# Kernel optimization log

Measured on AMD Instinct MI355X. Metric: run time of the kernel, lower is better.

The kernel has to match this reference:

```python
import jax, jax.numpy as jnp
import numpy as np

N_NODES = 100000
N_EDGES = 1600000
D_IN = 128
HID = 128
E_CH = 16


def setup_inputs() -> dict:
    key = jax.random.key(0)
    ks = jax.random.split(key, 16)

    def glorot(k, shape):
        fan_in, fan_out = shape[0], shape[1]
        lim = jnp.sqrt(6.0 / (fan_in + fan_out))
        return jax.random.uniform(k, shape, jnp.float32, -lim, lim)

    inp = {
        "x": jax.random.normal(ks[0], (N_NODES, D_IN), jnp.float32),
        "edge_index": jax.random.randint(ks[1], (2, N_EDGES), 0, N_NODES, jnp.int32),
        "edge_attr": jax.random.normal(ks[2], (N_EDGES, E_CH), jnp.float32),
        # SAGEConv layer 0: lin_l (neighbor agg, with bias), lin_r (root, no bias)
        "Wl0": glorot(ks[3], (D_IN, HID)),
        "Wr0": glorot(ks[4], (D_IN, HID)),
        "b0": jnp.zeros((HID,), jnp.float32),
        # SAGEConv layer 1
        "Wl1": glorot(ks[5], (HID, HID)),
        "Wr1": glorot(ks[6], (HID, HID)),
        "b1": jnp.zeros((HID,), jnp.float32),
        # classifier MLP: (2*HID + E_CH) -> 128 -> 64 -> 1
        "Wc1": glorot(ks[7], (2 * HID + E_CH, 128)),
        "bc1": jnp.zeros((128,), jnp.float32),
        "Wc2": glorot(ks[8], (128, 64)),
        "bc2": jnp.zeros((64,), jnp.float32),
        "Wc3": glorot(ks[9], (64, 1)),
        "bc3": jnp.zeros((1,), jnp.float32),
    }
    return inp


def _sage_conv(x, src, dst, Wl, Wr, b):
    # PyG SAGEConv (aggr='mean'): out = lin_l(mean_j x_j) + lin_r(x_i)
    # messages flow src -> dst
    msg_sum = jax.ops.segment_sum(x[src], dst, num_segments=N_NODES)  # [N, D]
    deg = jax.ops.segment_sum(jnp.ones((src.shape[0],), x.dtype), dst,
                              num_segments=N_NODES)                   # [N]
    agg = msg_sum / jnp.maximum(deg, 1.0)[:, None]  # mean; isolated nodes -> 0
    return agg @ Wl + b + x @ Wr


def reference(x, edge_index, edge_attr,
              Wl0, Wr0, b0, Wl1, Wr1, b1,
              Wc1, bc1, Wc2, bc2, Wc3, bc3):
    src, dst = edge_index[0], edge_index[1]
    # encode: two SAGEConv layers, each followed by ReLU (dropout is identity at eval)
    h = jax.nn.relu(_sage_conv(x, src, dst, Wl0, Wr0, b0))
    h = jax.nn.relu(_sage_conv(h, src, dst, Wl1, Wr1, b1))
    # edge classifier: gather endpoint embeddings, concat edge features
    feat = jnp.concatenate([h[src], h[dst], edge_attr], axis=-1)  # [E, 2H+EC]
    z = jax.nn.relu(feat @ Wc1 + bc1)
    z = jax.nn.relu(z @ Wc2 + bc2)
    logits = (z @ Wc3 + bc3).reshape(-1)  # [E]
    return jax.nn.sigmoid(logits)
```

## Files before the change

kernel.cpp:

```cpp
#include <hip/hip_runtime.h>
#include <hip/hip_bf16.h>
#include <math.h>

#define NN 100000
#define NE 1600000
#define NBLK 391

typedef __bf16 bf16x8 __attribute__((ext_vector_type(8)));
typedef float f32x4 __attribute__((ext_vector_type(4)));

union BF8 { bf16x8 v; unsigned short u[8]; };

static __device__ __forceinline__ unsigned short f2bf(float f) {
  unsigned int u = __float_as_uint(f);
  unsigned int r = u + 0x7fffu + ((u >> 16) & 1u);
  return (unsigned short)(r >> 16);
}
static __device__ __forceinline__ f32x4 zero4() {
  f32x4 z = {0.f, 0.f, 0.f, 0.f}; return z;
}
static __device__ __forceinline__ bf16x8 zerobf8() {
  BF8 t;
  #pragma unroll
  for (int j = 0; j < 8; ++j) t.u[j] = 0;
  return t.v;
}
static __device__ __forceinline__ bf16x8 cvt8(float4 v0, float4 v1, float s) {
  BF8 t;
  t.u[0]=f2bf(v0.x*s); t.u[1]=f2bf(v0.y*s); t.u[2]=f2bf(v0.z*s); t.u[3]=f2bf(v0.w*s);
  t.u[4]=f2bf(v1.x*s); t.u[5]=f2bf(v1.y*s); t.u[6]=f2bf(v1.z*s); t.u[7]=f2bf(v1.w*s);
  return t.v;
}

__global__ void prep_swizzle(const float* __restrict__ Wl0, const float* __restrict__ Wr0,
                             const float* __restrict__ Wl1, const float* __restrict__ Wr1,
                             const float* __restrict__ Wc1, const float* __restrict__ Wc2,
                             __hip_bfloat16* __restrict__ swz) {
  int gid = blockIdx.x * 256 + threadIdx.x;
  if (gid >= 110592) return;
  int id = gid;
  const float* A; const float* B = nullptr; int KC, Nc, Ksrc;
  if (id < 32768)        { KC = 8; Nc = 128; Ksrc = 256; A = Wl0; B = Wr0; }
  else if (id < 65536)   { id -= 32768; KC = 8; Nc = 128; Ksrc = 256; A = Wl1; B = Wr1; }
  else if (id < 102400)  { id -= 65536; KC = 9; Nc = 128; Ksrc = 272; A = Wc1; }
  else                   { id -= 102400; KC = 4; Nc = 64;  Ksrc = 128; A = Wc2; }
  int j = id & 7, lane = (id >> 3) & 63, rest = id >> 9;
  int c = rest % KC, t = rest / KC;
  int k = c * 32 + (lane >> 4) * 8 + j;
  int n = t * 16 + (lane & 15);
  float v = 0.f;
  if (k < Ksrc) {
    if (B && k >= 128) v = B[(k - 128) * Nc + n];
    else               v = A[k * Nc + n];
  }
  unsigned short* o = (unsigned short*)swz;
  o[gid] = f2bf(v);
}

__global__ void deg_count(const int* __restrict__ ei, int* __restrict__ degCnt) {
  int e = blockIdx.x * 256 + threadIdx.x;
  atomicAdd(&degCnt[ei[NE + e]], 1);
}

__global__ void scan_block_sums(const int* __restrict__ degCnt, int* __restrict__ blockSums) {
  __shared__ int red[4];
  int i = blockIdx.x * 256 + threadIdx.x;
  int v = (i < NN) ? degCnt[i] : 0;
  #pragma unroll
  for (int off = 32; off; off >>= 1) v += __shfl_down(v, off, 64);
  if ((threadIdx.x & 63) == 0) red[threadIdx.x >> 6] = v;
  __syncthreads();
  if (threadIdx.x == 0) blockSums[blockIdx.x] = red[0] + red[1] + red[2] + red[3];
}

__global__ void scan_partials(const int* __restrict__ blockSums, int* __restrict__ blockOff) {
  __shared__ int lds[512];
  int t = threadIdx.x;
  int v = (t < NBLK) ? blockSums[t] : 0;
  lds[t] = v; __syncthreads();
  #pragma unroll
  for (int off = 1; off < 512; off <<= 1) {
    int a = (t >= off) ? lds[t - off] : 0;
    __syncthreads();
    lds[t] += a;
    __syncthreads();
  }
  if (t < NBLK) blockOff[t] = lds[t] - v;
}

__global__ void scan_write(const int* __restrict__ degCnt, const int* __restrict__ blockOff,
                           int* __restrict__ rowPtr, int* __restrict__ cursor) {
  __shared__ int lds[256];
  int t = threadIdx.x;
  int i = blockIdx.x * 256 + t;
  int v = (i < NN) ? degCnt[i] : 0;
  lds[t] = v; __syncthreads();
  #pragma unroll
  for (int off = 1; off < 256; off <<= 1) {
    int a = (t >= off) ? lds[t - off] : 0;
    __syncthreads();
    lds[t] += a;
    __syncthreads();
  }
  if (i < NN) {
    int excl = blockOff[blockIdx.x] + lds[t] - v;
    rowPtr[i] = excl;
    cursor[i] = excl;
  }
}

__global__ void csr_fill(const int* __restrict__ ei, int* __restrict__ cursor,
                         int* __restrict__ csrSrc) {
  int e = blockIdx.x * 256 + threadIdx.x;
  int s = ei[e], d = ei[NE + e];
  int idx = atomicAdd(&cursor[d], 1);
  csrSrc[idx] = s;
}

__global__ __launch_bounds__(256, 8)
void gather_agg(const float* __restrict__ xf, const __hip_bfloat16* __restrict__ xb,
                const int* __restrict__ csrSrc, const int* __restrict__ rowPtr,
                const int* __restrict__ degCnt, __hip_bfloat16* __restrict__ msgOut) {
  int n = blockIdx.x * 4 + (threadIdx.x >> 6);
  int c2 = threadIdx.x & 63;
  if (n >= NN) return;
  int rp = rowPtr[n], dg = degCnt[n];
  float acc0 = 0.f, acc1 = 0.f;
  if (xf) {
    for (int i = 0; i < dg; ++i) {
      int s = csrSrc[rp + i];
      float2 v = *(const float2*)(xf + (size_t)s * 128 + c2 * 2);
      acc0 += v.x; acc1 += v.y;
    }
  } else {
    for (int i = 0; i < dg; ++i) {
      int s = csrSrc[rp + i];
      unsigned int u = *(const unsigned int*)(xb + (size_t)s * 128 + c2 * 2);
      acc0 += __uint_as_float(u << 16);
      acc1 += __uint_as_float(u & 0xffff0000u);
    }
  }
  float r = 1.f / fmaxf((float)dg, 1.f);
  unsigned int p = (unsigned int)f2bf(acc0 * r) | ((unsigned int)f2bf(acc1 * r) << 16);
  *(unsigned int*)((unsigned short*)msgOut + (size_t)n * 128 + c2 * 2) = p;
}

__global__ __launch_bounds__(256, 2)
void node_gemm(const __hip_bfloat16* __restrict__ msgB,
               const float* __restrict__ selfF32, const __hip_bfloat16* __restrict__ selfB16,
               const __hip_bfloat16* __restrict__ swzW, const float* __restrict__ bias,
               __hip_bfloat16* __restrict__ hOut) {
  const int tid = threadIdx.x, w = tid >> 6, lane = tid & 63;
  const int l15 = lane & 15, quad = lane >> 4;
  const int nBase = blockIdx.x * 256 + w * 64;

  int row[4];
  #pragma unroll
  for (int t = 0; t < 4; ++t) {
    int n = nBase + t * 16 + l15;
    if (n > NN - 1) n = NN - 1;
    row[t] = n;
  }

  f32x4 acc[8][4];
  #pragma unroll
  for (int mt = 0; mt < 8; ++mt)
    #pragma unroll
    for (int nt = 0; nt < 4; ++nt) acc[mt][nt] = zero4();

  #pragma unroll
  for (int c = 0; c < 8; ++c) {
    bf16x8 bfr[4];
    if (c < 4) {
      #pragma unroll
      for (int nt = 0; nt < 4; ++nt)
        bfr[nt] = *(const bf16x8*)(msgB + (size_t)row[nt] * 128 + c * 32 + quad * 8);
    } else {
      int cc = (c - 4) * 32 + quad * 8;
      if (selfF32) {
        #pragma unroll
        for (int nt = 0; nt < 4; ++nt) {
          const float4* p = (const float4*)(selfF32 + (size_t)row[nt] * 128 + cc);
          bfr[nt] = cvt8(p[0], p[1], 1.f);
        }
      } else {
        #pragma unroll
        for (int nt = 0; nt < 4; ++nt)
          bfr[nt] = *(const bf16x8*)(selfB16 + (size_t)row[nt] * 128 + cc);
      }
    }
    bf16x8 afr[8];
    #pragma unroll
    for (int mt = 0; mt < 8; ++mt)
      afr[mt] = *(const bf16x8*)(swzW + ((mt * 8 + c) * 64 + lane) * 8);
    #pragma unroll
    for (int mt = 0; mt < 8; ++mt)
      #pragma unroll
      for (int nt = 0; nt < 4; ++nt)
        acc[mt][nt] = __builtin_amdgcn_mfma_f32_16x16x32_bf16(afr[mt], bfr[nt], acc[mt][nt], 0, 0, 0);
  }

  #pragma unroll
  for (int mt = 0; mt < 8; ++mt) {
    const float4 b4 = *(const float4*)(bias + mt * 16 + quad * 4);
    #pragma unroll
    for (int nt = 0; nt < 4; ++nt) {
      int n = nBase + nt * 16 + l15;
      if (n < NN) {
        ushort4 p;
        p.x = f2bf(fmaxf(acc[mt][nt][0] + b4.x, 0.f));
        p.y = f2bf(fmaxf(acc[mt][nt][1] + b4.y, 0.f));
        p.z = f2bf(fmaxf(acc[mt][nt][2] + b4.z, 0.f));
        p.w = f2bf(fmaxf(acc[mt][nt][3] + b4.w, 0.f));
        *(ushort4*)(hOut + (size_t)n * 128 + mt * 16 + quad * 4) = p;
      }
    }
  }
}

__global__ __launch_bounds__(256, 2)
void edge_mlp(const __hip_bfloat16* __restrict__ h1, const int* __restrict__ ei,
              const float* __restrict__ ea,
              const __hip_bfloat16* __restrict__ swzWc1, const __hip_bfloat16* __restrict__ swzWc2,
              const float* __restrict__ Wc3, const float* __restrict__ bc1,
              const float* __restrict__ bc2, const float* __restrict__ bc3,
              float* __restrict__ out) {
  __shared__ char lds[4 * 64 * 288];
  const int tid = threadIdx.x, w = tid >> 6, lane = tid & 63;
  const int l15 = lane & 15, quad = lane >> 4;
  const int eBase = blockIdx.x * 256 + w * 64;
  char* zbuf = lds + w * (64 * 288);

  int eRow[4], srcOff[4], dstOff[4];
  #pragma unroll
  for (int t = 0; t < 4; ++t) {
    int e = eBase + t * 16 + l15;
    eRow[t] = e;
    srcOff[t] = ei[e] * 128;
    dstOff[t] = ei[NE + e] * 128;
  }

  f32x4 acc[8][4];
  #pragma unroll
  for (int mt = 0; mt < 8; ++mt)
    #pragma unroll
    for (int nt = 0; nt < 4; ++nt) acc[mt][nt] = zero4();

  #pragma unroll
  for (int c = 0; c < 9; ++c) {
    bf16x8 bfr[4];
    if (c < 4) {
      #pragma unroll
      for (int nt = 0; nt < 4; ++nt)
        bfr[nt] = *(const bf16x8*)(h1 + srcOff[nt] + c * 32 + quad * 8);
    } else if (c < 8) {
      #pragma unroll
      for (int nt = 0; nt < 4; ++nt)
        bfr[nt] = *(const bf16x8*)(h1 + dstOff[nt] + (c - 4) * 32 + quad * 8);
    } else {
      #pragma unroll
      for (int nt = 0; nt < 4; ++nt) {
        if (quad < 2) {
          const float4* p = (const float4*)(ea + (size_t)eRow[nt] * 16 + quad * 8);
          bfr[nt] = cvt8(p[0], p[1], 1.f);
        } else {
          bfr[nt] = zerobf8();
        }
      }
    }
    bf16x8 afr[8];
    #pragma unroll
    for (int mt = 0; mt < 8; ++mt)
      afr[mt] = *(const bf16x8*)(swzWc1 + ((mt * 9 + c) * 64 + lane) * 8);
    #pragma unroll
    for (int mt = 0; mt < 8; ++mt)
      #pragma unroll
      for (int nt = 0; nt < 4; ++nt)
        acc[mt][nt] = __builtin_amdgcn_mfma_f32_16x16x32_bf16(afr[mt], bfr[nt], acc[mt][nt], 0, 0, 0);
  }

  #pragma unroll
  for (int mt = 0; mt < 8; ++mt) {
    const float4 b4 = *(const float4*)(bc1 + mt * 16 + quad * 4);
    #pragma unroll
    for (int nt = 0; nt < 4; ++nt) {
      int er = nt * 16 + l15;
      ushort4 p;
      p.x = f2bf(fmaxf(acc[mt][nt][0] + b4.x, 0.f));
      p.y = f2bf(fmaxf(acc[mt][nt][1] + b4.y, 0.f));
      p.z = f2bf(fmaxf(acc[mt][nt][2] + b4.z, 0.f));
      p.w = f2bf(fmaxf(acc[mt][nt][3] + b4.w, 0.f));
      *(ushort4*)(zbuf + er * 288 + (mt * 16 + quad * 4) * 2) = p;
    }
  }

  f32x4 acc2[4][4];
  #pragma unroll
  for (int mt = 0; mt < 4; ++mt)
    #pragma unroll
    for (int nt = 0; nt < 4; ++nt) acc2[mt][nt] = zero4();

  #pragma unroll
  for (int c = 0; c < 4; ++c) {
    bf16x8 bfr[4];
    #pragma unroll
    for (int nt = 0; nt < 4; ++nt)
      bfr[nt] = *(const bf16x8*)(zbuf + (nt * 16 + l15) * 288 + (c * 32 + quad * 8) * 2);
    bf16x8 afr[4];
    #pragma unroll
    for (int mt = 0; mt < 4; ++mt)
      afr[mt] = *(const bf16x8*)(swzWc2 + ((mt * 4 + c) * 64 + lane) * 8);
    #pragma unroll
    for (int mt = 0; mt < 4; ++mt)
      #pragma unroll
      for (int nt = 0; nt < 4; ++nt)
        acc2[mt][nt] = __builtin_amdgcn_mfma_f32_16x16x32_bf16(afr[mt], bfr[nt], acc2[mt][nt], 0, 0, 0);
  }

  #pragma unroll
  for (int mt = 0; mt < 4; ++mt) {
    const float4 b4 = *(const float4*)(bc2 + mt * 16 + quad * 4);
    #pragma unroll
    for (int nt = 0; nt < 4; ++nt) {
      int er = nt * 16 + l15;
      ushort4 p;
      p.x = f2bf(fmaxf(acc2[mt][nt][0] + b4.x, 0.f));
      p.y = f2bf(fmaxf(acc2[mt][nt][1] + b4.y, 0.f));
      p.z = f2bf(fmaxf(acc2[mt][nt][2] + b4.z, 0.f));
      p.w = f2bf(fmaxf(acc2[mt][nt][3] + b4.w, 0.f));
      *(ushort4*)(zbuf + er * 272 + (mt * 16 + quad * 4) * 2) = p;
    }
  }

  float a3 = bc3[0];
  #pragma unroll
  for (int k2 = 0; k2 < 32; ++k2) {
    unsigned int u = *(const unsigned int*)(zbuf + lane * 272 + k2 * 4);
    float v0 = __uint_as_float(u << 16);
    float v1 = __uint_as_float(u & 0xffff0000u);
    a3 += v0 * Wc3[2 * k2] + v1 * Wc3[2 * k2 + 1];
  }
  out[eBase + lane] = 1.f / (1.f + __expf(-a3));
}

extern "C" void kernel_launch(void* const* d_in, const int* in_sizes, int n_in,
                              void* d_out, int out_size, void* d_ws, size_t ws_size,
                              hipStream_t stream) {
  const float* x   = (const float*)d_in[0];
  const int*   ei  = (const int*)d_in[1];
  const float* ea  = (const float*)d_in[2];
  const float* Wl0 = (const float*)d_in[3];
  const float* Wr0 = (const float*)d_in[4];
  const float* b0  = (const float*)d_in[5];
  const float* Wl1 = (const float*)d_in[6];
  const float* Wr1 = (const float*)d_in[7];
  const float* b1  = (const float*)d_in[8];
  const float* Wc1 = (const float*)d_in[9];
  const float* bc1 = (const float*)d_in[10];
  const float* Wc2 = (const float*)d_in[11];
  const float* bc2 = (const float*)d_in[12];
  const float* Wc3 = (const float*)d_in[13];
  const float* bc3 = (const float*)d_in[14];
  float* out = (float*)d_out;

  char* ws = (char*)d_ws;
  int* degCnt   = (int*)(ws + 0);
  int* rowPtr   = (int*)(ws + 400000);
  int* cursor   = (int*)(ws + 800000);
  int* blockSums= (int*)(ws + 1200000);
  int* blockOff = (int*)(ws + 1202048);
  int* csrSrc   = (int*)(ws + 1204096);
  __hip_bfloat16* msgB = (__hip_bfloat16*)(ws + 7604096);
  __hip_bfloat16* h0b  = (__hip_bfloat16*)(ws + 33204096);
  __hip_bfloat16* h1b  = (__hip_bfloat16*)(ws + 58804096);
  __hip_bfloat16* swz  = (__hip_bfloat16*)(ws + 84404096);

  hipMemsetAsync(degCnt, 0, 400000, stream);
  prep_swizzle<<<432, 256, 0, stream>>>(Wl0, Wr0, Wl1, Wr1, Wc1, Wc2, swz);

  deg_count<<<NE / 256, 256, 0, stream>>>(ei, degCnt);
  scan_block_sums<<<NBLK, 256, 0, stream>>>(degCnt, blockSums);
  scan_partials<<<1, 512, 0, stream>>>(blockSums, blockOff);
  scan_write<<<NBLK, 256, 0, stream>>>(degCnt, blockOff, rowPtr, cursor);
  csr_fill<<<NE / 256, 256, 0, stream>>>(ei, cursor, csrSrc);

  gather_agg<<<NN / 4, 256, 0, stream>>>(x, nullptr, csrSrc, rowPtr, degCnt, msgB);
  node_gemm<<<(NN + 255) / 256, 256, 0, stream>>>(msgB, x, nullptr, swz, b0, h0b);

  gather_agg<<<NN / 4, 256, 0, stream>>>(nullptr, h0b, csrSrc, rowPtr, degCnt, msgB);
  node_gemm<<<(NN + 255) / 256, 256, 0, stream>>>(msgB, nullptr, h0b, swz + 32768, b1, h1b);

  edge_mlp<<<NE / 256, 256, 0, stream>>>(h1b, ei, ea, swz + 65536, swz + 102400,
                                         Wc3, bc1, bc2, bc3, out);
}
```

Before: 1.010 ms.

## Convert x to bf16 up front, split gather across half-waves, shrink edge MLP tiles

Adds a pre-pass that converts x to bf16 so the first gather and the root GEMM read half the bytes. The gather now has each half-wave walk alternate neighbours with 4-channel loads, then combines the halves with a shuffle, which doubles the loads in flight per node. The edge MLP processes 32 edges per wave instead of 64, which cuts accumulator registers so occupancy can rise from 2 to 4 blocks. It also pads the LDS row stride to reduce bank conflicts and splits the final dot product across half-waves. In exchange it adds an extra kernel pass over x and rounds x to bf16 before the first aggregation, and the h1 buffer is reused for the converted x.

```diff
diff --git a/kernel.cpp b/kernel.cpp
--- a/kernel.cpp
+++ b/kernel.cpp
@@ -5,6 +5,7 @@
 #define NN 100000
 #define NE 1600000
 #define NBLK 391
+#define ZSTRIDE 296
 
 typedef __bf16 bf16x8 __attribute__((ext_vector_type(8)));
 typedef float f32x4 __attribute__((ext_vector_type(4)));
@@ -57,6 +58,14 @@
   o[gid] = f2bf(v);
 }
 
+__global__ void x_to_bf16(const float* __restrict__ x, __hip_bfloat16* __restrict__ xb) {
+  int i = blockIdx.x * 256 + threadIdx.x;
+  float4 v = ((const float4*)x)[i];
+  ushort4 p;
+  p.x = f2bf(v.x); p.y = f2bf(v.y); p.z = f2bf(v.z); p.w = f2bf(v.w);
+  ((ushort4*)xb)[i] = p;
+}
+
 __global__ void deg_count(const int* __restrict__ ei, int* __restrict__ degCnt) {
   int e = blockIdx.x * 256 + threadIdx.x;
   atomicAdd(&degCnt[ei[NE + e]], 1);
@@ -118,36 +127,40 @@
 }
 
 __global__ __launch_bounds__(256, 8)
-void gather_agg(const float* __restrict__ xf, const __hip_bfloat16* __restrict__ xb,
+void gather_agg(const __hip_bfloat16* __restrict__ xb,
                 const int* __restrict__ csrSrc, const int* __restrict__ rowPtr,
                 const int* __restrict__ degCnt, __hip_bfloat16* __restrict__ msgOut) {
   int n = blockIdx.x * 4 + (threadIdx.x >> 6);
-  int c2 = threadIdx.x & 63;
+  int lane = threadIdx.x & 63;
+  int half = lane >> 5;
+  int c4 = lane & 31;
   if (n >= NN) return;
   int rp = rowPtr[n], dg = degCnt[n];
-  float acc0 = 0.f, acc1 = 0.f;
-  if (xf) {
-    for (int i = 0; i < dg; ++i) {
-      int s = csrSrc[rp + i];
-      float2 v = *(const float2*)(xf + (size_t)s * 128 + c2 * 2);
-      acc0 += v.x; acc1 += v.y;
-    }
-  } else {
-    for (int i = 0; i < dg; ++i) {
-      int s = csrSrc[rp + i];
-      unsigned int u = *(const unsigned int*)(xb + (size_t)s * 128 + c2 * 2);
-      acc0 += __uint_as_float(u << 16);
-      acc1 += __uint_as_float(u & 0xffff0000u);
-    }
-  }
-  float r = 1.f / fmaxf((float)dg, 1.f);
-  unsigned int p = (unsigned int)f2bf(acc0 * r) | ((unsigned int)f2bf(acc1 * r) << 16);
-  *(unsigned int*)((unsigned short*)msgOut + (size_t)n * 128 + c2 * 2) = p;
+  float a0 = 0.f, a1 = 0.f, a2 = 0.f, a3 = 0.f;
+  for (int i = half; i < dg; i += 2) {
+    int s = csrSrc[rp + i];
+    uint2 u = *(const uint2*)((const unsigned short*)xb + (size_t)s * 128 + c4 * 4);
+    a0 += __uint_as_float(u.x << 16);
+    a1 += __uint_as_float(u.x & 0xffff0000u);
+    a2 += __uint_as_float(u.y << 16);
+    a3 += __uint_as_float(u.y & 0xffff0000u);
+  }
+  a0 += __shfl_xor(a0, 32);
+  a1 += __shfl_xor(a1, 32);
+  a2 += __shfl_xor(a2, 32);
+  a3 += __shfl_xor(a3, 32);
+  if (half == 0) {
+    float r = 1.f / fmaxf((float)dg, 1.f);
+    ushort4 p;
+    p.x = f2bf(a0 * r); p.y = f2bf(a1 * r);
+    p.z = f2bf(a2 * r); p.w = f2bf(a3 * r);
+    *(ushort4*)((unsigned short*)msgOut + (size_t)n * 128 + c4 * 4) = p;
+  }
 }
 
 __global__ __launch_bounds__(256, 2)
 void node_gemm(const __hip_bfloat16* __restrict__ msgB,
-               const float* __restrict__ selfF32, const __hip_bfloat16* __restrict__ selfB16,
+               const __hip_bfloat16* __restrict__ selfB16,
                const __hip_bfloat16* __restrict__ swzW, const float* __restrict__ bias,
                __hip_bfloat16* __restrict__ hOut) {
   const int tid = threadIdx.x, w = tid >> 6, lane = tid & 63;
@@ -176,18 +189,9 @@
       for (int nt = 0; nt < 4; ++nt)
         bfr[nt] = *(const bf16x8*)(msgB + (size_t)row[nt] * 128 + c * 32 + quad * 8);
     } else {
-      int cc = (c - 4) * 32 + quad * 8;
-      if (selfF32) {
-        #pragma unroll
-        for (int nt = 0; nt < 4; ++nt) {
-          const float4* p = (const float4*)(selfF32 + (size_t)row[nt] * 128 + cc);
-          bfr[nt] = cvt8(p[0], p[1], 1.f);
-        }
-      } else {
-        #pragma unroll
-        for (int nt = 0; nt < 4; ++nt)
-          bfr[nt] = *(const bf16x8*)(selfB16 + (size_t)row[nt] * 128 + cc);
-      }
+      #pragma unroll
+      for (int nt = 0; nt < 4; ++nt)
+        bfr[nt] = *(const bf16x8*)(selfB16 + (size_t)row[nt] * 128 + (c - 4) * 32 + quad * 8);
     }
     bf16x8 afr[8];
     #pragma unroll
@@ -218,48 +222,48 @@
   }
 }
 
-__global__ __launch_bounds__(256, 2)
+__global__ __launch_bounds__(256, 4)
 void edge_mlp(const __hip_bfloat16* __restrict__ h1, const int* __restrict__ ei,
               const float* __restrict__ ea,
               const __hip_bfloat16* __restrict__ swzWc1, const __hip_bfloat16* __restrict__ swzWc2,
               const float* __restrict__ Wc3, const float* __restrict__ bc1,
               const float* __restrict__ bc2, const float* __restrict__ bc3,
               float* __restrict__ out) {
-  __shared__ char lds[4 * 64 * 288];
+  __shared__ char lds[4 * 32 * ZSTRIDE];
   const int tid = threadIdx.x, w = tid >> 6, lane = tid & 63;
   const int l15 = lane & 15, quad = lane >> 4;
-  const int eBase = blockIdx.x * 256 + w * 64;
-  char* zbuf = lds + w * (64 * 288);
-
-  int eRow[4], srcOff[4], dstOff[4];
-  #pragma unroll
-  for (int t = 0; t < 4; ++t) {
+  const int eBase = blockIdx.x * 128 + w * 32;
+  char* zbuf = lds + w * (32 * ZSTRIDE);
+
+  int eRow[2], srcOff[2], dstOff[2];
+  #pragma unroll
+  for (int t = 0; t < 2; ++t) {
     int e = eBase + t * 16 + l15;
     eRow[t] = e;
     srcOff[t] = ei[e] * 128;
     dstOff[t] = ei[NE + e] * 128;
   }
 
-  f32x4 acc[8][4];
+  f32x4 acc[8][2];
   #pragma unroll
   for (int mt = 0; mt < 8; ++mt)
     #pragma unroll
-    for (int nt = 0; nt < 4; ++nt) acc[mt][nt] = zero4();
+    for (int nt = 0; nt < 2; ++nt) acc[mt][nt] = zero4();
 
   #pragma unroll
   for (int c = 0; c < 9; ++c) {
-    bf16x8 bfr[4];
+    bf16x8 bfr[2];
     if (c < 4) {
       #pragma unroll
-      for (int nt = 0; nt < 4; ++nt)
+      for (int nt = 0; nt < 2; ++nt)
         bfr[nt] = *(const bf16x8*)(h1 + srcOff[nt] + c * 32 + quad * 8);
     } else if (c < 8) {
       #pragma unroll
-      for (int nt = 0; nt < 4; ++nt)
+      for (int nt = 0; nt < 2; ++nt)
         bfr[nt] = *(const bf16x8*)(h1 + dstOff[nt] + (c - 4) * 32 + quad * 8);
     } else {
       #pragma unroll
-      for (int nt = 0; nt < 4; ++nt) {
+      for (int nt = 0; nt < 2; ++nt) {
         if (quad < 2) {
           const float4* p = (const float4*)(ea + (size_t)eRow[nt] * 16 + quad * 8);
           bfr[nt] = cvt8(p[0], p[1], 1.f);
@@ -275,7 +279,7 @@
     #pragma unroll
     for (int mt = 0; mt < 8; ++mt)
       #pragma unroll
-      for (int nt = 0; nt < 4; ++nt)
+      for (int nt = 0; nt < 2; ++nt)
         acc[mt][nt] = __builtin_amdgcn_mfma_f32_16x16x32_bf16(afr[mt], bfr[nt], acc[mt][nt], 0, 0, 0);
   }
 
@@ -283,29 +287,29 @@
   for (int mt = 0; mt < 8; ++mt) {
     const float4 b4 = *(const float4*)(bc1 + mt * 16 + quad * 4);
     #pragma unroll
-    for (int nt = 0; nt < 4; ++nt) {
+    for (int nt = 0; nt < 2; ++nt) {
       int er = nt * 16 + l15;
       ushort4 p;
       p.x = f2bf(fmaxf(acc[mt][nt][0] + b4.x, 0.f));
       p.y = f2bf(fmaxf(acc[mt][nt][1] + b4.y, 0.f));
       p.z = f2bf(fmaxf(acc[mt][nt][2] + b4.z, 0.f));
       p.w = f2bf(fmaxf(acc[mt][nt][3] + b4.w, 0.f));
-      *(ushort4*)(zbuf + er * 288 + (mt * 16 + quad * 4) * 2) = p;
-    }
-  }
-
-  f32x4 acc2[4][4];
+      *(ushort4*)(zbuf + er * ZSTRIDE + (mt * 16 + quad * 4) * 2) = p;
+    }
+  }
+
+  f32x4 acc2[4][2];
   #pragma unroll
   for (int mt = 0; mt < 4; ++mt)
     #pragma unroll
-    for (int nt = 0; nt < 4; ++nt) acc2[mt][nt] = zero4();
+    for (int nt = 0; nt < 2; ++nt) acc2[mt][nt] = zero4();
 
   #pragma unroll
   for (int c = 0; c < 4; ++c) {
-    bf16x8 bfr[4];
-    #pragma unroll
-    for (int nt = 0; nt < 4; ++nt)
-      bfr[nt] = *(const bf16x8*)(zbuf + (nt * 16 + l15) * 288 + (c * 32 + quad * 8) * 2);
+    bf16x8 bfr[2];
+    #pragma unroll
+    for (int nt = 0; nt < 2; ++nt)
+      bfr[nt] = *(const bf16x8*)(zbuf + (nt * 16 + l15) * ZSTRIDE + (c * 32 + quad * 8) * 2);
     bf16x8 afr[4];
     #pragma unroll
     for (int mt = 0; mt < 4; ++mt)
@@ -313,7 +317,7 @@
     #pragma unroll
     for (int mt = 0; mt < 4; ++mt)
       #pragma unroll
-      for (int nt = 0; nt < 4; ++nt)
+      for (int nt = 0; nt < 2; ++nt)
         acc2[mt][nt] = __builtin_amdgcn_mfma_f32_16x16x32_bf16(afr[mt], bfr[nt], acc2[mt][nt], 0, 0, 0);
   }
 
@@ -321,26 +325,32 @@
   for (int mt = 0; mt < 4; ++mt) {
     const float4 b4 = *(const float4*)(bc2 + mt * 16 + quad * 4);
     #pragma unroll
-    for (int nt = 0; nt < 4; ++nt) {
+    for (int nt = 0; nt < 2; ++nt) {
       int er = nt * 16 + l15;
       ushort4 p;
       p.x = f2bf(fmaxf(acc2[mt][nt][0] + b4.x, 0.f));
       p.y = f2bf(fmaxf(acc2[mt][nt][1] + b4.y, 0.f));
       p.z = f2bf(fmaxf(acc2[mt][nt][2] + b4.z, 0.f));
       p.w = f2bf(fmaxf(acc2[mt][nt][3] + b4.w, 0.f));
-      *(ushort4*)(zbuf + er * 272 + (mt * 16 + quad * 4) * 2) = p;
-    }
-  }
-
-  float a3 = bc3[0];
-  #pragma unroll
-  for (int k2 = 0; k2 < 32; ++k2) {
-    unsigned int u = *(const unsigned int*)(zbuf + lane * 272 + k2 * 4);
-    float v0 = __uint_as_float(u << 16);
-    float v1 = __uint_as_float(u & 0xffff0000u);
-    a3 += v0 * Wc3[2 * k2] + v1 * Wc3[2 * k2 + 1];
-  }
-  out[eBase + lane] = 1.f / (1.f + __expf(-a3));
+      *(ushort4*)(zbuf + er * ZSTRIDE + (mt * 16 + quad * 4) * 2) = p;
+    }
+  }
+
+  {
+    int e = lane & 31, half = lane >> 5;
+    float a3 = (half == 0) ? bc3[0] : 0.f;
+    #pragma unroll
+    for (int k2 = 0; k2 < 16; ++k2) {
+      unsigned int u = *(const unsigned int*)(zbuf + e * ZSTRIDE + half * 64 + k2 * 4);
+      float v0 = __uint_as_float(u << 16);
+      float v1 = __uint_as_float(u & 0xffff0000u);
+      const float2 wv = *(const float2*)(Wc3 + half * 32 + 2 * k2);
+      a3 += v0 * wv.x + v1 * wv.y;
+    }
+    a3 += __shfl_xor(a3, 32);
+    if (half == 0)
+      out[eBase + e] = 1.f / (1.f + __expf(-a3));
+  }
 }
 
 extern "C" void kernel_launch(void* const* d_in, const int* in_sizes, int n_in,
@@ -374,9 +384,11 @@
   __hip_bfloat16* h0b  = (__hip_bfloat16*)(ws + 33204096);
   __hip_bfloat16* h1b  = (__hip_bfloat16*)(ws + 58804096);
   __hip_bfloat16* swz  = (__hip_bfloat16*)(ws + 84404096);
+  __hip_bfloat16* xb = h1b;
 
   hipMemsetAsync(degCnt, 0, 400000, stream);
   prep_swizzle<<<432, 256, 0, stream>>>(Wl0, Wr0, Wl1, Wr1, Wc1, Wc2, swz);
+  x_to_bf16<<<12500, 256, 0, stream>>>(x, xb);
 
   deg_count<<<NE / 256, 256, 0, stream>>>(ei, degCnt);
   scan_block_sums<<<NBLK, 256, 0, stream>>>(degCnt, blockSums);
@@ -384,12 +396,12 @@
   scan_write<<<NBLK, 256, 0, stream>>>(degCnt, blockOff, rowPtr, cursor);
   csr_fill<<<NE / 256, 256, 0, stream>>>(ei, cursor, csrSrc);
 
-  gather_agg<<<NN / 4, 256, 0, stream>>>(x, nullptr, csrSrc, rowPtr, degCnt, msgB);
-  node_gemm<<<(NN + 255) / 256, 256, 0, stream>>>(msgB, x, nullptr, swz, b0, h0b);
-
-  gather_agg<<<NN / 4, 256, 0, stream>>>(nullptr, h0b, csrSrc, rowPtr, degCnt, msgB);
-  node_gemm<<<(NN + 255) / 256, 256, 0, stream>>>(msgB, nullptr, h0b, swz + 32768, b1, h1b);
-
-  edge_mlp<<<NE / 256, 256, 0, stream>>>(h1b, ei, ea, swz + 65536, swz + 102400,
+  gather_agg<<<NN / 4, 256, 0, stream>>>(xb, csrSrc, rowPtr, degCnt, msgB);
+  node_gemm<<<(NN + 255) / 256, 256, 0, stream>>>(msgB, xb, swz, b0, h0b);
+
+  gather_agg<<<NN / 4, 256, 0, stream>>>(h0b, csrSrc, rowPtr, degCnt, msgB);
+  node_gemm<<<(NN + 255) / 256, 256, 0, stream>>>(msgB, h0b, swz + 32768, b1, h1b);
+
+  edge_mlp<<<NE / 128, 256, 0, stream>>>(h1b, ei, ea, swz + 65536, swz + 102400,
                                          Wc3, bc1, bc2, bc3, out);
 }
```

After: 964.7 us. 4.5% less time.
